# Performance work log

Hardware: AMD Instinct MI355X
Metric: run time of the kernel (lower is better)

Reference implementation:

```python
import jax, jax.numpy as jnp
import numpy as np
from jax import lax

B, C, H, W = 64, 384, 28, 28
E, K, R = 3, 2, 8          # num_experts, top_k, lora rank
HID = 4 * C                # ConvNeXt MLP hidden
EPS = 1e-6
SCALING = 8.0 / 8.0        # alpha / r


def setup_inputs() -> dict:
    key = jax.random.key(0)
    ks = jax.random.split(key, 18)
    N = B * H * W
    f32 = jnp.float32
    inp = {
        "x": jax.random.normal(ks[0], (B, C, H, W), f32),
        "conv_w": jax.random.normal(ks[1], (C, 1, 7, 7), f32) * 0.05,
        "conv_b": jax.random.normal(ks[2], (C,), f32) * 0.02,
        "norm_g": 1.0 + jax.random.normal(ks[3], (C,), f32) * 0.02,
        "norm_b": jax.random.normal(ks[4], (C,), f32) * 0.02,
        "dom_g": jax.random.normal(ks[5], (E, C), f32) * 0.02,
        "dom_b": jax.random.normal(ks[6], (E, C), f32) * 0.02,
        "fc1_w": jax.random.normal(ks[7], (C, HID), f32) * (C ** -0.5),
        "fc1_b": jax.random.normal(ks[8], (HID,), f32) * 0.02,
        "fc2_w": jax.random.normal(ks[9], (HID, C), f32) * (HID ** -0.5),
        "fc2_b": jax.random.normal(ks[10], (C,), f32) * 0.02,
        "w_down": jax.random.normal(ks[11], (E, C, R), f32) * (C ** -0.5),
        "w_up": jax.random.normal(ks[12], (E, R, C), f32) * 0.02,
        "gamma": jax.random.normal(ks[13], (C,), f32) * 0.1,
        "routing_weights": jax.nn.softmax(jax.random.normal(ks[14], (B, E), f32), axis=-1),
        "topk_probs": jax.nn.softmax(jax.random.normal(ks[15], (N, K), f32), axis=-1),
        "topk_indices": jax.random.randint(ks[16], (N, K), 0, E),
    }
    return inp


def _forward(x, conv_w, conv_b, norm_g, norm_b, dom_g, dom_b,
             fc1_w, fc1_b, fc2_w, fc2_b, w_down, w_up, gamma,
             routing_weights, topk_probs, topk_indices):
    shortcut = x
    # depthwise 7x7 conv, NCHW, SAME padding
    y = lax.conv_general_dilated(
        x, conv_w, window_strides=(1, 1), padding=((3, 3), (3, 3)),
        feature_group_count=C,
        dimension_numbers=("NCHW", "OIHW", "NCHW"))
    y = y + conv_b[None, :, None, None]
    y = jnp.transpose(y, (0, 2, 3, 1))  # [B, H, W, C] channels-last path

    # ParallelMoELayerNorm: orig LN + sum_i w_i * LN_i(x). All LNs share eps,
    # so normalize once and fuse affine params per-sample.
    mu = jnp.mean(y, axis=-1, keepdims=True)
    var = jnp.mean(jnp.square(y - mu), axis=-1, keepdims=True)
    xhat = (y - mu) * lax.rsqrt(var + EPS)
    g_eff = norm_g[None, :] + routing_weights @ dom_g   # [B, C]
    b_eff = norm_b[None, :] + routing_weights @ dom_b   # [B, C]
    y = xhat * g_eff[:, None, None, :] + b_eff[:, None, None, :]

    # base ConvNeXt MLP (exact GELU, as torch nn.GELU)
    h = jax.nn.gelu(jnp.einsum("bhwc,cf->bhwf", y, fc1_w) + fc1_b,
                    approximate=False)
    orig_out = jnp.einsum("bhwf,fc->bhwc", h, fc2_w) + fc2_b

    # MoE LoRA: dense per-expert rank-8 compute, combined with top-k weights.
    # Equivalent math to the gather/matmul/scatter-add loop in the source.
    y_flat = y.reshape(-1, C)                                   # [N, C]
    down = jnp.einsum("nc,ecr->enr", y_flat, w_down)            # [E, N, R]
    up = jnp.einsum("enr,erc->enc", jax.nn.gelu(down, approximate=False), w_up)
    # combine weights: comb[n, e] = sum_k topk_probs[n, k] * (topk_indices[n,k]==e)
    comb = jnp.sum(jax.nn.one_hot(topk_indices, E, dtype=y.dtype)
                   * topk_probs[..., None], axis=1)             # [N, E]
    moe_out = jnp.einsum("enc,ne->nc", up * SCALING, comb)
    y = orig_out + moe_out.reshape(B, H, W, C)

    y = jnp.transpose(y, (0, 3, 1, 2))  # back to NCHW
    y = gamma[None, :, None, None] * y  # layer scale; drop_path = identity (eval)
    return y + shortcut


def reference(x, conv_w, conv_b, norm_g, norm_b, dom_g, dom_b,
              fc1_w, fc1_b, fc2_w, fc2_b, w_down, w_up, gamma,
              routing_weights, topk_probs, topk_indices):
    return _forward(x, conv_w, conv_b, norm_g, norm_b, dom_g, dom_b,
                    fc1_w, fc1_b, fc2_w, fc2_b, w_down, w_up, gamma,
                    routing_weights, topk_probs, topk_indices)
```

## Files before the change

### kernel.cpp

```cpp
#include <hip/hip_runtime.h>
#include <hip/hip_bf16.h>
#include <cstdint>
#include <cstddef>

constexpr int cB   = 64;
constexpr int cC   = 384;
constexpr int cH   = 28;
constexpr int cW   = 28;
constexpr int cHID = 1536;
constexpr int cNTOK = cB * cH * cW;
constexpr int cKP   = cHID + 64;

typedef __attribute__((ext_vector_type(8))) short bf16x8;
typedef __attribute__((ext_vector_type(4))) float f32x4;

__device__ __forceinline__ float gelu_f(float x) {
  float u = 1.5957691216057308f * x * (1.0f + 0.044715f * x * x);
  float e = __expf(-u);
  return x / (1.0f + e);
}

__device__ __forceinline__ float bf16_to_f(unsigned short s) {
  return __uint_as_float(((unsigned)s) << 16);
}
__device__ __forceinline__ unsigned short f_to_bf16(float v) {
  __hip_bfloat16 hb = __float2bfloat16(v);
  return *reinterpret_cast<unsigned short*>(&hb);
}

__device__ __forceinline__ void gload_lds16(const void* g, void* l) {
  __builtin_amdgcn_global_load_lds(
      (const __attribute__((address_space(1))) unsigned int*)g,
      (__attribute__((address_space(3))) unsigned int*)l, 16, 0, 0);
}

__device__ __forceinline__ int xcd_remap(int b, int nwg) {
  int qn = nwg >> 3, rm = nwg & 7;
  int xcd = b & 7, off = b >> 3;
  return (xcd < rm) ? xcd * (qn + 1) + off
                    : rm * (qn + 1) + (xcd - rm) * qn + off;
}

__global__ __launch_bounds__(256) void prep_eff(
    const float* __restrict__ ng, const float* __restrict__ nb,
    const float* __restrict__ dg, const float* __restrict__ db,
    const float* __restrict__ rw, float* __restrict__ geff, float* __restrict__ beff) {
  int i = blockIdx.x * 256 + threadIdx.x;
  if (i >= cB * cC) return;
  int b = i / cC, c = i - b * cC;
  float g = ng[c], bb = nb[c];
#pragma unroll
  for (int e = 0; e < 3; ++e) {
    float r = rw[b * 3 + e];
    g += r * dg[e * cC + c];
    bb += r * db[e * cC + c];
  }
  geff[i] = g;
  beff[i] = bb;
}

__global__ __launch_bounds__(256) void transpose_bf16(
    const float* __restrict__ w, __hip_bfloat16* __restrict__ wt, int R0, int C0) {
  __shared__ float t[64][65];
  int c0 = blockIdx.x * 64, r0 = blockIdx.y * 64;
  for (int i = threadIdx.x; i < 64 * 64; i += 256) {
    int r = i >> 6, c = i & 63;
    t[r][c] = w[(size_t)(r0 + r) * C0 + c0 + c];
  }
  __syncthreads();
  for (int i = threadIdx.x; i < 64 * 64; i += 256) {
    int c = i >> 6, r = i & 63;
    wt[(size_t)(c0 + c) * R0 + r0 + r] = __float2bfloat16(t[r][c]);
  }
}

__global__ __launch_bounds__(256) void build_fc2t(
    const float* __restrict__ fc2w, const float* __restrict__ wu,
    __hip_bfloat16* __restrict__ fc2t) {
  int i = blockIdx.x * 256 + threadIdx.x;
  if (i >= cC * cKP) return;
  int c = i / cKP, k = i - c * cKP;
  float v = 0.f;
  if (k < cHID) v = fc2w[(size_t)k * cC + c];
  else {
    int j = k - cHID;
    if (j < 24) v = wu[(size_t)(j >> 3) * 8 * cC + (size_t)(j & 7) * cC + c];
  }
  fc2t[i] = __float2bfloat16(v);
}

__global__ __launch_bounds__(256) void build_wdt(
    const float* __restrict__ wd, __hip_bfloat16* __restrict__ wdt) {
  int i = blockIdx.x * 256 + threadIdx.x;
  if (i >= 32 * cC) return;
  int j = i / cC, c = i - j * cC;
  float v = 0.f;
  if (j < 24) v = wd[(size_t)(j >> 3) * cC * 8 + (size_t)c * 8 + (j & 7)];
  wdt[i] = __float2bfloat16(v);
}

constexpr int cPL = 4;
__global__ __launch_bounds__(128) void conv_dw(
    const float* __restrict__ x, const float* __restrict__ cw,
    const float* __restrict__ cb, __hip_bfloat16* __restrict__ out) {
  int pb = blockIdx.x * cPL;
  int c0 = pb % cC;
  __shared__ __align__(16) float tile[cPL][34][38];
  __shared__ float wsm[cPL][49];
  const int tid = threadIdx.x;

  float2 z2 = {0.f, 0.f};
  for (int i = tid; i < cPL * 34 * 38 / 2; i += 128)
    ((float2*)tile)[i] = z2;
  __syncthreads();

  for (int i = tid; i < cPL * 196; i += 128) {
    int p = i / 196, q = i - p * 196;
    int r = q / 7, cl = (q - r * 7) * 4;
    float4 v = *(const float4*)&x[(size_t)(pb + p) * 784 + r * 28 + cl];
    float* dst = &tile[p][r + 3][cl + 4];
    *(float2*)dst = make_float2(v.x, v.y);
    *(float2*)(dst + 2) = make_float2(v.z, v.w);
  }
  for (int i = tid; i < cPL * 49; i += 128) {
    int p = i / 49, k = i - p * 49;
    wsm[p][k] = cw[(size_t)(c0 + p) * 49 + k];
  }
  __syncthreads();

  if (tid < cPL * 28) {
    int p = tid / 28, r = tid - p * 28;
    float acc[28];
    float cbv = cb[c0 + p];
#pragma unroll
    for (int w = 0; w < 28; ++w) acc[w] = cbv;
    for (int dh = 0; dh < 7; ++dh) {
      float rowv[36];
      const float* rp = &tile[p][r + dh][0];
#pragma unroll
      for (int k = 0; k < 18; ++k)
        ((float2*)rowv)[k] = *(const float2*)(rp + k * 2);
      float w7[7];
#pragma unroll
      for (int dw = 0; dw < 7; ++dw) w7[dw] = wsm[p][dh * 7 + dw];
#pragma unroll
      for (int w = 0; w < 28; ++w)
#pragma unroll
        for (int dw = 0; dw < 7; ++dw)
          acc[w] += rowv[w + dw + 1] * w7[dw];
    }
    unsigned short* op = (unsigned short*)out + (size_t)(pb + p) * 784 + r * 28;
#pragma unroll
    for (int k = 0; k < 7; ++k) {
      ushort4 s;
      s.x = f_to_bf16(acc[k * 4 + 0]);
      s.y = f_to_bf16(acc[k * 4 + 1]);
      s.z = f_to_bf16(acc[k * 4 + 2]);
      s.w = f_to_bf16(acc[k * 4 + 3]);
      *(ushort4*)&op[k * 4] = s;
    }
  }
}

__global__ __launch_bounds__(256) void ln_affine(
    const __hip_bfloat16* __restrict__ convout, const float* __restrict__ geff,
    const float* __restrict__ beff, __hip_bfloat16* __restrict__ y) {
  int bh = blockIdx.x;
  int b = bh / cH;
  int hrow = bh - b * cH;
  __shared__ float t[cC * 29];
  const unsigned short* src =
      (const unsigned short*)convout + (size_t)b * cC * (cH * cW) + (size_t)hrow * cW;
  for (int i = threadIdx.x; i < cC * 7; i += 256) {
    int c = i / 7, wq = (i - c * 7) * 4;
    ushort4 v = *(const ushort4*)&src[(size_t)c * (cH * cW) + wq];
    t[c * 29 + wq + 0] = bf16_to_f(v.x);
    t[c * 29 + wq + 1] = bf16_to_f(v.y);
    t[c * 29 + wq + 2] = bf16_to_f(v.z);
    t[c * 29 + wq + 3] = bf16_to_f(v.w);
  }
  __syncthreads();
  int wave = threadIdx.x >> 6, lane = threadIdx.x & 63;
  const float* gp = geff + (size_t)b * cC;
  const float* bp = beff + (size_t)b * cC;
  for (int w = wave; w < cW; w += 4) {
    float v[6], s = 0.f, s2 = 0.f;
#pragma unroll
    for (int j = 0; j < 6; ++j) {
      v[j] = t[(lane + 64 * j) * 29 + w];
      s += v[j];
      s2 += v[j] * v[j];
    }
#pragma unroll
    for (int d = 32; d; d >>= 1) {
      s += __shfl_xor(s, d);
      s2 += __shfl_xor(s2, d);
    }
    float mu = s * (1.0f / cC);
    float var = s2 * (1.0f / cC) - mu * mu;
    float rstd = rsqrtf(var + 1e-6f);
    size_t n = (size_t)bh * cW + w;
#pragma unroll
    for (int j = 0; j < 6; ++j) {
      int c = lane + 64 * j;
      float val = (v[j] - mu) * rstd * gp[c] + bp[c];
      y[n * cC + c] = __float2bfloat16(val);
    }
  }
}

template <int DO_GELU>
__global__ __launch_bounds__(256) void gemm_bt(
    const __hip_bfloat16* __restrict__ A, int lda,
    const __hip_bfloat16* __restrict__ Bt,
    const float* __restrict__ bias,
    __hip_bfloat16* __restrict__ Cb, int ldc,
    int M, int N, int K, int NT_N) {
  __shared__ __align__(16) char smem[40960];
  const int bid = xcd_remap(blockIdx.x, gridDim.x);
  const int gsz = 8 * NT_N;
  const int g = bid / gsz;
  const int q = bid - g * gsz;
  const int mi = g * 8 + q / NT_N;
  const int ni = q - (q / NT_N) * NT_N;
  const int m0 = mi * 128, n0 = ni * 128;

  const int tid = threadIdx.x;
  const int lane = tid & 63;
  const int wid = tid >> 6;
  const int wm = wid >> 1, wn = wid & 1;
  const int l15 = lane & 15, lq = lane >> 4;

  const __hip_bfloat16* srcA[2];
  const __hip_bfloat16* srcB[2];
  int dstA[2], dstB[2];
#pragma unroll
  for (int a = 0; a < 2; ++a) {
    int gu = a * 256 + tid;
    int row = gu >> 2, pu = gu & 3;
    int u = pu ^ (row & 3);
    srcA[a] = &A[(size_t)(m0 + row) * lda + u * 8];
    srcB[a] = &Bt[(size_t)(n0 + row) * K + u * 8];
    dstA[a] = gu * 16;
    dstB[a] = 16384 + gu * 16;
  }

#define STAGE(BUF)                                                   \
  do {                                                               \
    _Pragma("unroll") for (int a = 0; a < 2; ++a) {                  \
      gload_lds16(srcA[a], smem + (BUF) * 8192 + dstA[a]);           \
      gload_lds16(srcB[a], smem + (BUF) * 8192 + dstB[a]);           \
      srcA[a] += 32; srcB[a] += 32;                                  \
    }                                                                \
  } while (0)

  int roA[4], roB[4];
#pragma unroll
  for (int i = 0; i < 4; ++i) {
    int rowA = wm * 64 + i * 16 + l15;
    int rowB = wn * 64 + i * 16 + l15;
    roA[i] = rowA * 64 + (lq ^ (rowA & 3)) * 16;
    roB[i] = 16384 + rowB * 64 + (lq ^ (rowB & 3)) * 16;
  }

  const int nt = K >> 5;

  STAGE(0);
  __syncthreads();

  f32x4 acc[4][4] = {};
  int cur = 0;
  for (int t = 0; t < nt; ++t, cur ^= 1) {
    if (t + 1 < nt) STAGE(cur ^ 1);
    const char* base = smem + cur * 8192;
    bf16x8 af[4], bf[4];
#pragma unroll
    for (int i = 0; i < 4; ++i) af[i] = *(const bf16x8*)(base + roA[i]);
#pragma unroll
    for (int i = 0; i < 4; ++i) bf[i] = *(const bf16x8*)(base + roB[i]);
#pragma unroll
    for (int i = 0; i < 4; ++i)
#pragma unroll
      for (int j = 0; j < 4; ++j)
        acc[i][j] = __builtin_amdgcn_mfma_f32_16x16x32_bf16(af[i], bf[j], acc[i][j], 0, 0, 0);
    __syncthreads();
  }
#undef STAGE

  float* cst = (float*)smem;
  for (int hf = 0; hf < 2; ++hf) {
    if (hf) __syncthreads();
    if (wn == hf) {
#pragma unroll
      for (int i = 0; i < 4; ++i) {
        int row = wm * 64 + i * 16 + lq * 4;
#pragma unroll
        for (int j = 0; j < 4; ++j) {
          int col = j * 16 + l15;
          float bv = bias[n0 + hf * 64 + col];
#pragma unroll
          for (int r = 0; r < 4; ++r) {
            float vv = acc[i][j][r] + bv;
            if (DO_GELU) vv = gelu_f(vv);
            cst[(row + r) * 72 + col] = vv;
          }
        }
      }
    }
    __syncthreads();
#pragma unroll
    for (int s = 0; s < 4; ++s) {
      int slot = s * 256 + tid;
      int row = slot >> 3, c8 = slot & 7;
      const float* rp = &cst[row * 72 + c8 * 8];
      bf16x8 v;
#pragma unroll
      for (int e = 0; e < 8; ++e)
        v[e] = (short)f_to_bf16(rp[e]);
      *(bf16x8*)&Cb[(size_t)(m0 + row) * ldc + n0 + hf * 64 + c8 * 8] = v;
    }
  }
}

__global__ __launch_bounds__(256) void lora_down(
    const __hip_bfloat16* __restrict__ y,
    const __hip_bfloat16* __restrict__ wdt,
    const float* __restrict__ probs,
    const int* __restrict__ inds,
    __hip_bfloat16* __restrict__ h) {
  __shared__ __align__(16) __hip_bfloat16 As[2][128 * 32];
  __shared__ __align__(16) __hip_bfloat16 Bsm[32 * 384];
  const int tid = threadIdx.x, lane = tid & 63, wid = tid >> 6;
  const int n0 = blockIdx.x * 128;

  for (int i = tid; i < 32 * 384 / 8; i += 256)
    ((bf16x8*)Bsm)[i] = ((const bf16x8*)wdt)[i];

  const int base0 = wid * 2048, base1 = base0 + 1024;
  const int off0 = base0 + lane * 16, off1 = base1 + lane * 16;
  const int row0 = off0 >> 6, col0 = (off0 >> 1) & 31;
  const int row1 = off1 >> 6, col1 = (off1 >> 1) & 31;
  const __hip_bfloat16* pa0 = &y[(size_t)(n0 + row0) * cC + col0];
  const __hip_bfloat16* pa1 = &y[(size_t)(n0 + row1) * cC + col1];

  const int nt = cC >> 5;
  gload_lds16(pa0, (char*)As[0] + base0);
  gload_lds16(pa1, (char*)As[0] + base1);
  pa0 += 32; pa1 += 32;
  __syncthreads();

  f32x4 acc[2][2] = {};
  int cur = 0;
  for (int t = 0; t < nt; ++t, cur ^= 1) {
    if (t + 1 < nt) {
      gload_lds16(pa0, (char*)As[cur ^ 1] + base0);
      gload_lds16(pa1, (char*)As[cur ^ 1] + base1);
      pa0 += 32; pa1 += 32;
    }
    int kt = t * 32;
    bf16x8 af[2], bfr[2];
#pragma unroll
    for (int i = 0; i < 2; ++i)
      af[i] = *(const bf16x8*)&As[cur][(wid * 32 + i * 16 + (lane & 15)) * 32 + (lane >> 4) * 8];
#pragma unroll
    for (int j = 0; j < 2; ++j)
      bfr[j] = *(const bf16x8*)&Bsm[(j * 16 + (lane & 15)) * 384 + kt + (lane >> 4) * 8];
#pragma unroll
    for (int i = 0; i < 2; ++i)
#pragma unroll
      for (int j = 0; j < 2; ++j)
        acc[i][j] = __builtin_amdgcn_mfma_f32_16x16x32_bf16(af[i], bfr[j], acc[i][j], 0, 0, 0);
    __syncthreads();
  }

#pragma unroll
  for (int i = 0; i < 2; ++i) {
#pragma unroll
    for (int j = 0; j < 2; ++j) {
      int colb = j * 16 + (lane & 15);
#pragma unroll
      for (int r = 0; r < 4; ++r) {
        int n = n0 + wid * 32 + i * 16 + (lane >> 4) * 4 + r;
        float zv = 0.f;
        if (colb < 24) {
          int e = colb >> 3;
          float comb = 0.f;
          if (inds[(size_t)n * 2] == e)     comb += probs[(size_t)n * 2];
          if (inds[(size_t)n * 2 + 1] == e) comb += probs[(size_t)n * 2 + 1];
          zv = comb * gelu_f(acc[i][j][r]);
        }
        h[(size_t)n * cKP + cHID + colb] = __float2bfloat16(zv);
        h[(size_t)n * cKP + cHID + 32 + colb] = __float2bfloat16(0.f);
      }
    }
  }
}

__global__ __launch_bounds__(256) void final_out(
    const __hip_bfloat16* __restrict__ tmp, const float* __restrict__ x,
    const float* __restrict__ gamma, float* __restrict__ out) {
  int bh = blockIdx.x;
  int b = bh / cH, hrow = bh - b * cH;
  __shared__ float t[cW * 385];
  const __hip_bfloat16* src = tmp + (size_t)bh * cW * cC;
  for (int i = threadIdx.x; i < cW * cC / 8; i += 256) {
    bf16x8 v = ((const bf16x8*)src)[i];
    int base = i * 8;
    int w = base / cC, c = base - w * cC;
#pragma unroll
    for (int k = 0; k < 8; ++k)
      t[w * 385 + c + k] = bf16_to_f((unsigned short)v[k]);
  }
  __syncthreads();
  const float* xb = x + (size_t)b * cC * (cH * cW) + (size_t)hrow * cW;
  float* ob = out + (size_t)b * cC * (cH * cW) + (size_t)hrow * cW;
  for (int i = threadIdx.x; i < cC * cW; i += 256) {
    int c = i / cW, w = i - c * cW;
    ob[(size_t)c * (cH * cW) + w] = gamma[c] * t[w * 385 + c] + xb[(size_t)c * (cH * cW) + w];
  }
}

extern "C" void kernel_launch(void* const* d_in, const int* in_sizes, int n_in,
                              void* d_out, int out_size, void* d_ws, size_t ws_size,
                              hipStream_t stream) {
  const float* x      = (const float*)d_in[0];
  const float* conv_w = (const float*)d_in[1];
  const float* conv_b = (const float*)d_in[2];
  const float* norm_g = (const float*)d_in[3];
  const float* norm_b = (const float*)d_in[4];
  const float* dom_g  = (const float*)d_in[5];
  const float* dom_b  = (const float*)d_in[6];
  const float* fc1_w  = (const float*)d_in[7];
  const float* fc1_b  = (const float*)d_in[8];
  const float* fc2_w  = (const float*)d_in[9];
  const float* fc2_b  = (const float*)d_in[10];
  const float* w_down = (const float*)d_in[11];
  const float* w_up   = (const float*)d_in[12];
  const float* gamma  = (const float*)d_in[13];
  const float* rw     = (const float*)d_in[14];
  const float* tkp    = (const float*)d_in[15];
  const int*   tki    = (const int*)d_in[16];
  float* out = (float*)d_out;

  char* ws = (char*)d_ws;
  __hip_bfloat16* y      = (__hip_bfloat16*)(ws + 0);
  __hip_bfloat16* tmpb   = (__hip_bfloat16*)(ws + 38535168);
  char*           hslot  = ws + 77070336;
  __hip_bfloat16* h      = (__hip_bfloat16*)hslot;
  __hip_bfloat16* convb  = (__hip_bfloat16*)hslot;
  __hip_bfloat16* fc1t   = (__hip_bfloat16*)(ws + 237633536);
  __hip_bfloat16* fc2t   = (__hip_bfloat16*)(ws + 238813184);
  __hip_bfloat16* wdt    = (__hip_bfloat16*)(ws + 240041984);
  float*          geff   = (float*)(ws + 240066560);
  float*          beff   = (float*)(ws + 240164864);

  prep_eff<<<(cB * cC + 255) / 256, 256, 0, stream>>>(norm_g, norm_b, dom_g, dom_b, rw, geff, beff);
  transpose_bf16<<<dim3(cHID / 64, cC / 64), 256, 0, stream>>>(fc1_w, fc1t, cC, cHID);
  build_fc2t<<<(cC * cKP + 255) / 256, 256, 0, stream>>>(fc2_w, w_up, fc2t);
  build_wdt<<<(32 * cC + 255) / 256, 256, 0, stream>>>(w_down, wdt);
  conv_dw<<<cB * cC / cPL, 128, 0, stream>>>(x, conv_w, conv_b, convb);
  ln_affine<<<cB * cH, 256, 0, stream>>>(convb, geff, beff, y);

  const int NTM = cNTOK / 128;
  gemm_bt<1><<<NTM * (cHID / 128), 256, 0, stream>>>(
      y, cC, fc1t, fc1_b, h, cKP, cNTOK, cHID, cC, cHID / 128);
  lora_down<<<cNTOK / 128, 256, 0, stream>>>(y, wdt, tkp, tki, h);
  gemm_bt<0><<<NTM * (cC / 128), 256, 0, stream>>>(
      h, cKP, fc2t, fc2_b, tmpb, cC, cNTOK, cC, cKP, cC / 128);

  final_out<<<cB * cH, 256, 0, stream>>>(tmpb, x, gamma, out);
}
```

Before: 451.8 us.

## Chunk MLP over two token halves, drop LDS swizzle, bf16 epilogue staging

Splits the fc1/lora/fc2 sequence into two token chunks that reuse a half-size hidden buffer, so the intermediate activations are more likely to stay in the MI355X's large last-level cache between the GEMMs. The GEMM now stages its epilogue in bf16 rather than fp32 in LDS, cutting shared memory to 32KB to allow higher occupancy. It also removes the XOR swizzle on the LDS tiles, which risks bank conflicts, and halves the conv block to 64 threads with 2 planes each. The trade-off is extra kernel launches and smaller GEMM grids per chunk.

```diff
diff --git a/kernel.cpp b/kernel.cpp
--- a/kernel.cpp
+++ b/kernel.cpp
@@ -10,6 +10,8 @@
 constexpr int cHID = 1536;
 constexpr int cNTOK = cB * cH * cW;
 constexpr int cKP   = cHID + 64;
+constexpr int cCH   = 2;
+constexpr int cMR   = cNTOK / cCH;
 
 typedef __attribute__((ext_vector_type(8))) short bf16x8;
 typedef __attribute__((ext_vector_type(4))) float f32x4;
@@ -99,8 +101,8 @@
   wdt[i] = __float2bfloat16(v);
 }
 
-constexpr int cPL = 4;
-__global__ __launch_bounds__(128) void conv_dw(
+constexpr int cPL = 2;
+__global__ __launch_bounds__(64) void conv_dw(
     const float* __restrict__ x, const float* __restrict__ cw,
     const float* __restrict__ cb, __hip_bfloat16* __restrict__ out) {
   int pb = blockIdx.x * cPL;
@@ -110,11 +112,11 @@
   const int tid = threadIdx.x;
 
   float2 z2 = {0.f, 0.f};
-  for (int i = tid; i < cPL * 34 * 38 / 2; i += 128)
+  for (int i = tid; i < cPL * 34 * 19; i += 64)
     ((float2*)tile)[i] = z2;
   __syncthreads();
 
-  for (int i = tid; i < cPL * 196; i += 128) {
+  for (int i = tid; i < cPL * 196; i += 64) {
     int p = i / 196, q = i - p * 196;
     int r = q / 7, cl = (q - r * 7) * 4;
     float4 v = *(const float4*)&x[(size_t)(pb + p) * 784 + r * 28 + cl];
@@ -122,7 +124,7 @@
     *(float2*)dst = make_float2(v.x, v.y);
     *(float2*)(dst + 2) = make_float2(v.z, v.w);
   }
-  for (int i = tid; i < cPL * 49; i += 128) {
+  for (int i = tid; i < cPL * 49; i += 64) {
     int p = i / 49, k = i - p * 49;
     wsm[p][k] = cw[(size_t)(c0 + p) * 49 + k];
   }
@@ -216,7 +218,8 @@
     const float* __restrict__ bias,
     __hip_bfloat16* __restrict__ Cb, int ldc,
     int M, int N, int K, int NT_N) {
-  __shared__ __align__(16) char smem[40960];
+  __shared__ __align__(16) char smem[32768];
+
   const int bid = xcd_remap(blockIdx.x, gridDim.x);
   const int gsz = 8 * NT_N;
   const int g = bid / gsz;
@@ -237,10 +240,9 @@
 #pragma unroll
   for (int a = 0; a < 2; ++a) {
     int gu = a * 256 + tid;
-    int row = gu >> 2, pu = gu & 3;
-    int u = pu ^ (row & 3);
-    srcA[a] = &A[(size_t)(m0 + row) * lda + u * 8];
-    srcB[a] = &Bt[(size_t)(n0 + row) * K + u * 8];
+    int row = gu >> 2, c8 = gu & 3;
+    srcA[a] = &A[(size_t)(m0 + row) * lda + c8 * 8];
+    srcB[a] = &Bt[(size_t)(n0 + row) * K + c8 * 8];
     dstA[a] = gu * 16;
     dstB[a] = 16384 + gu * 16;
   }
@@ -257,10 +259,8 @@
   int roA[4], roB[4];
 #pragma unroll
   for (int i = 0; i < 4; ++i) {
-    int rowA = wm * 64 + i * 16 + l15;
-    int rowB = wn * 64 + i * 16 + l15;
-    roA[i] = rowA * 64 + (lq ^ (rowA & 3)) * 16;
-    roB[i] = 16384 + rowB * 64 + (lq ^ (rowB & 3)) * 16;
+    roA[i] = (wm * 64 + i * 16 + l15) * 64 + lq * 16;
+    roB[i] = 16384 + (wn * 64 + i * 16 + l15) * 64 + lq * 16;
   }
 
   const int nt = K >> 5;
@@ -287,13 +287,13 @@
   }
 #undef STAGE
 
-  float* cst = (float*)smem;
+  unsigned short* cb16 = (unsigned short*)smem;
   for (int hf = 0; hf < 2; ++hf) {
     if (hf) __syncthreads();
     if (wn == hf) {
 #pragma unroll
       for (int i = 0; i < 4; ++i) {
-        int row = wm * 64 + i * 16 + lq * 4;
+        int rowb = wm * 64 + i * 16 + lq * 4;
 #pragma unroll
         for (int j = 0; j < 4; ++j) {
           int col = j * 16 + l15;
@@ -302,7 +302,7 @@
           for (int r = 0; r < 4; ++r) {
             float vv = acc[i][j][r] + bv;
             if (DO_GELU) vv = gelu_f(vv);
-            cst[(row + r) * 72 + col] = vv;
+            cb16[(rowb + r) * 72 + col] = f_to_bf16(vv);
           }
         }
       }
@@ -312,11 +312,7 @@
     for (int s = 0; s < 4; ++s) {
       int slot = s * 256 + tid;
       int row = slot >> 3, c8 = slot & 7;
-      const float* rp = &cst[row * 72 + c8 * 8];
-      bf16x8 v;
-#pragma unroll
-      for (int e = 0; e < 8; ++e)
-        v[e] = (short)f_to_bf16(rp[e]);
+      bf16x8 v = *(const bf16x8*)&cb16[row * 72 + c8 * 8];
       *(bf16x8*)&Cb[(size_t)(m0 + row) * ldc + n0 + hf * 64 + c8 * 8] = v;
     }
   }
@@ -448,25 +444,29 @@
   char*           hslot  = ws + 77070336;
   __hip_bfloat16* h      = (__hip_bfloat16*)hslot;
   __hip_bfloat16* convb  = (__hip_bfloat16*)hslot;
-  __hip_bfloat16* fc1t   = (__hip_bfloat16*)(ws + 237633536);
-  __hip_bfloat16* fc2t   = (__hip_bfloat16*)(ws + 238813184);
-  __hip_bfloat16* wdt    = (__hip_bfloat16*)(ws + 240041984);
-  float*          geff   = (float*)(ws + 240066560);
-  float*          beff   = (float*)(ws + 240164864);
+  __hip_bfloat16* fc1t   = (__hip_bfloat16*)(ws + 157351936);
+  __hip_bfloat16* fc2t   = (__hip_bfloat16*)(ws + 158531584);
+  __hip_bfloat16* wdt    = (__hip_bfloat16*)(ws + 159760384);
+  float*          geff   = (float*)(ws + 159784960);
+  float*          beff   = (float*)(ws + 159883264);
 
   prep_eff<<<(cB * cC + 255) / 256, 256, 0, stream>>>(norm_g, norm_b, dom_g, dom_b, rw, geff, beff);
   transpose_bf16<<<dim3(cHID / 64, cC / 64), 256, 0, stream>>>(fc1_w, fc1t, cC, cHID);
   build_fc2t<<<(cC * cKP + 255) / 256, 256, 0, stream>>>(fc2_w, w_up, fc2t);
   build_wdt<<<(32 * cC + 255) / 256, 256, 0, stream>>>(w_down, wdt);
-  conv_dw<<<cB * cC / cPL, 128, 0, stream>>>(x, conv_w, conv_b, convb);
+  conv_dw<<<cB * cC / cPL, 64, 0, stream>>>(x, conv_w, conv_b, convb);
   ln_affine<<<cB * cH, 256, 0, stream>>>(convb, geff, beff, y);
 
-  const int NTM = cNTOK / 128;
-  gemm_bt<1><<<NTM * (cHID / 128), 256, 0, stream>>>(
-      y, cC, fc1t, fc1_b, h, cKP, cNTOK, cHID, cC, cHID / 128);
-  lora_down<<<cNTOK / 128, 256, 0, stream>>>(y, wdt, tkp, tki, h);
-  gemm_bt<0><<<NTM * (cC / 128), 256, 0, stream>>>(
-      h, cKP, fc2t, fc2_b, tmpb, cC, cNTOK, cC, cKP, cC / 128);
+  const int NTM = cMR / 128;
+  for (int ch = 0; ch < cCH; ++ch) {
+    const __hip_bfloat16* ych = y + (size_t)ch * cMR * cC;
+    gemm_bt<1><<<NTM * (cHID / 128), 256, 0, stream>>>(
+        ych, cC, fc1t, fc1_b, h, cKP, cMR, cHID, cC, cHID / 128);
+    lora_down<<<cMR / 128, 256, 0, stream>>>(
+        ych, wdt, tkp + (size_t)ch * cMR * 2, tki + (size_t)ch * cMR * 2, h);
+    gemm_bt<0><<<NTM * (cC / 128), 256, 0, stream>>>(
+        h, cKP, fc2t, fc2_b, tmpb + (size_t)ch * cMR * cC, cC, cMR, cC, cKP, cC / 128);
+  }
 
   final_out<<<cB * cH, 256, 0, stream>>>(tmpb, x, gamma, out);
 }
```

Result: faster. 437.3 us (-3.2%).
